# Performance work log

Measured on AMD Instinct MI355X. Metric: run time of the kernel, lower is better.

The kernel has to match this reference:

```python
import jax, jax.numpy as jnp
import numpy as np

N, D, H, L, B, DFF = 100000, 256, 8, 64, 4096, 1024
HD = D // H  # head_dim
EPS = 1e-5


def _xavier(k, shape):
    lim = (6.0 / (shape[0] + shape[1])) ** 0.5
    return jax.random.uniform(k, shape, jnp.float32, -lim, lim)


def setup_inputs() -> dict:
    key = jax.random.key(0)
    ks = jax.random.split(key, 12)
    batch = jax.random.randint(ks[0], (B,), 0, N)
    nei_idx = jax.random.randint(ks[1], (B, L), 0, N)
    # faithful to neis_ = [[k] + neighbor[k] ...]: self node is first neighbor
    nei_idx = nei_idx.at[:, 0].set(batch)
    lengths = jax.random.randint(ks[2], (B,), 1, L + 1)
    nei_mask = jnp.arange(L)[None, :] >= lengths[:, None]  # True = NaN padding
    embeddings = jax.random.normal(ks[3], (N, D), jnp.float32)
    return {
        "batch": batch, "nei_idx": nei_idx, "nei_mask": nei_mask,
        "embeddings": embeddings,
        "Wq": _xavier(ks[4], (D, D)), "bq": jnp.zeros((D,), jnp.float32),
        "Wk": _xavier(ks[5], (D, D)), "bk": jnp.zeros((D,), jnp.float32),
        "Wv": _xavier(ks[6], (D, D)), "bv": jnp.zeros((D,), jnp.float32),
        "Wo": _xavier(ks[7], (D, D)), "bo": jnp.zeros((D,), jnp.float32),
        "W1": _xavier(ks[8], (D, DFF)), "b1": jnp.zeros((DFF,), jnp.float32),
        "W2": _xavier(ks[9], (DFF, D)), "b2": jnp.zeros((D,), jnp.float32),
        "ln1_w": jnp.ones((D,), jnp.float32), "ln1_b": jnp.zeros((D,), jnp.float32),
        "ln2_w": jnp.ones((D,), jnp.float32), "ln2_b": jnp.zeros((D,), jnp.float32),
    }


def _layer_norm(y, w, b):
    mu = y.mean(-1, keepdims=True)
    var = ((y - mu) ** 2).mean(-1, keepdims=True)
    return (y - mu) / jnp.sqrt(var + EPS) * w + b


def reference(batch, nei_idx, nei_mask, embeddings,
              Wq, bq, Wk, bk, Wv, bv, Wo, bo,
              W1, b1, W2, b2, ln1_w, ln1_b, ln2_w, ln2_b):
    x = embeddings[batch]        # [B, D]  query-node embeddings
    nei = embeddings[nei_idx]    # [B, L, D] gathered (padded) neighbor embeds
    q = ((x @ Wq + bq) * (HD ** -0.5)).reshape(B, H, HD)
    k = (nei @ Wk + bk).reshape(B, L, H, HD)
    v = (nei @ Wv + bv).reshape(B, L, H, HD)
    scores = jnp.einsum('bhd,blhd->bhl', q, k)          # single-query attn
    scores = jnp.where(nei_mask[:, None, :], -jnp.inf, scores)
    att = jax.nn.softmax(scores, axis=-1)               # [B, H, L]
    attout = jnp.einsum('bhl,blhd->bhd', att, v).reshape(B, D) @ Wo + bo
    s = _layer_norm(x + attout, ln1_w, ln1_b)
    # note: original applies relu after BOTH linear1 and linear2
    f = jax.nn.relu(jax.nn.relu(s @ W1 + b1) @ W2 + b2)
    return _layer_norm(s + f, ln2_w, ln2_b)
```

## Files before the change

kernel.cpp:

```cpp
#include <hip/hip_runtime.h>
#include <hip/hip_bf16.h>
#include <math.h>

#define BQ   4096
#define D    256
#define NH   8
#define HD   32
#define LN_  64
#define DFF  1024
#define EPSV 1e-5f
#define QSCALE 0.17677669529663687f

typedef __attribute__((ext_vector_type(8))) short short8;
typedef __attribute__((ext_vector_type(4))) float f32x4;

#define ESWZ(row, byte) ((byte) ^ (((row) & 7) << 4))

__device__ __forceinline__ float wave_sum(float v){
#pragma unroll
  for (int off = 32; off; off >>= 1) v += __shfl_xor(v, off, 64);
  return v;
}
__device__ __forceinline__ unsigned short f2bf(float f){
  __hip_bfloat16 h = __float2bfloat16(f);
  unsigned short r; __builtin_memcpy(&r, &h, 2); return r;
}
__device__ __forceinline__ unsigned pk2(float a, float b){
  __hip_bfloat162 h = __float22bfloat162_rn(make_float2(a, b));
  unsigned r; __builtin_memcpy(&r, &h, 4); return r;
}

__global__ __launch_bounds__(256) void k_prep(
    const float* __restrict__ Wq, const float* __restrict__ Wk,
    const float* __restrict__ Wv, const float* __restrict__ Wo,
    const float* __restrict__ W1, const float* __restrict__ W2,
    const float* __restrict__ bq, const float* __restrict__ bv,
    const float* __restrict__ bo,
    const int* __restrict__ batch, const float* __restrict__ emb,
    const unsigned int* __restrict__ maskw,
    unsigned short* __restrict__ W1t, unsigned short* __restrict__ W2t,
    unsigned short* __restrict__ Mt, unsigned short* __restrict__ Gt,
    float* __restrict__ pb, float* __restrict__ bo2,
    float* __restrict__ X, unsigned short* __restrict__ Xb,
    int* __restrict__ flagsArr){
  __shared__ float smem[4224];
  const int bid = blockIdx.x;
  const int tid = threadIdx.x;

  if (bid < 128){
    const float* src; unsigned short* dst; int K, N, t0;
    if (bid < 64){ src = W1; dst = W1t; K = 256;  N = 1024; t0 = bid; }
    else         { src = W2; dst = W2t; K = 1024; N = 256;  t0 = bid - 64; }
    const int ntx = N / 64;
    const int k0 = (t0 / ntx) * 64, n0 = (t0 % ntx) * 64;
    float (*Ts)[65] = (float(*)[65])smem;
    {
      int r = tid >> 2, c4 = (tid & 3) * 16;
#pragma unroll
      for (int i = 0; i < 4; i++)
        *(float4*)&Ts[r][c4 + i * 4] = *(const float4*)(src + (size_t)(k0 + r) * N + n0 + c4 + i * 4);
    }
    __syncthreads();
    {
      int n = tid >> 2, kc = (tid & 3) * 16;
      unsigned int pk[8];
#pragma unroll
      for (int i = 0; i < 8; i++)
        pk[i] = pk2(Ts[kc + 2 * i][n], Ts[kc + 2 * i + 1][n]);
      unsigned short* orow = dst + (size_t)(n0 + n) * K + k0 + kc;
      *(uint4*)(orow)     = *(uint4*)&pk[0];
      *(uint4*)(orow + 8) = *(uint4*)&pk[4];
    }
    return;
  }
  if (bid < 256){
    int t0 = bid - 128;
    int hd0 = (t0 & 31) * 64, c0 = (t0 >> 5) * 64;
    int h = hd0 >> 8, d0 = hd0 & 255;
    float (*WqS)[33] = (float(*)[33])smem;
    float (*WkS)[33] = (float(*)[33])(smem + 64 * 33);
#pragma unroll
    for (int s = 0; s < 2; s++){
      int idx = tid + s * 256;
      int row = idx >> 3, c4 = (idx & 7) * 4;
      *(float4*)&WqS[row][c4] = *(const float4*)(Wq + (size_t)(c0 + row) * 256 + h * 32 + c4);
      *(float4*)&WkS[row][c4] = *(const float4*)(Wk + (size_t)(d0 + row) * 256 + h * 32 + c4);
    }
    __syncthreads();
    int jo = (tid >> 4) * 4, io = (tid & 15) * 4;
    float acc[4][4];
#pragma unroll
    for (int j = 0; j < 4; j++)
#pragma unroll
      for (int i = 0; i < 4; i++) acc[j][i] = 0.f;
#pragma unroll
    for (int t = 0; t < 32; t++){
#pragma unroll
      for (int j = 0; j < 4; j++){
        float kv = WkS[jo + j][t];
#pragma unroll
        for (int i = 0; i < 4; i++) acc[j][i] = fmaf(kv, WqS[io + i][t], acc[j][i]);
      }
    }
#pragma unroll
    for (int j = 0; j < 4; j++){
      uint2 o;
      o.x = pk2(acc[j][0] * QSCALE, acc[j][1] * QSCALE);
      o.y = pk2(acc[j][2] * QSCALE, acc[j][3] * QSCALE);
      *(uint2*)(Mt + (size_t)(hd0 + jo + j) * 256 + c0 + io) = o;
    }
    if (c0 == 0 && tid < 64){
      float s = 0.f;
#pragma unroll
      for (int t = 0; t < 32; t++) s = fmaf(WkS[tid][t], bq[h * 32 + t], s);
      pb[hd0 + tid] = s * QSCALE;
    }
    return;
  }
  if (bid < 384){
    int t0 = bid - 256;
    int hd0 = (t0 & 31) * 64, n0 = (t0 >> 5) * 64;
    int h = hd0 >> 8, d0 = hd0 & 255;
    float (*WvS)[33] = (float(*)[33])smem;
    float (*WoS)[65] = (float(*)[65])(smem + 64 * 33);
#pragma unroll
    for (int s = 0; s < 2; s++){
      int idx = tid + s * 256;
      int row = idx >> 3, c4 = (idx & 7) * 4;
      *(float4*)&WvS[row][c4] = *(const float4*)(Wv + (size_t)(d0 + row) * 256 + h * 32 + c4);
      int row2 = idx >> 4, c42 = (idx & 15) * 4;
      *(float4*)&WoS[row2][c42] = *(const float4*)(Wo + (size_t)(h * 32 + row2) * 256 + n0 + c42);
    }
    __syncthreads();
    int jo = (tid >> 4) * 4, io = (tid & 15) * 4;
    float acc[4][4];
#pragma unroll
    for (int i = 0; i < 4; i++)
#pragma unroll
      for (int j = 0; j < 4; j++) acc[i][j] = 0.f;
#pragma unroll
    for (int t = 0; t < 32; t++){
#pragma unroll
      for (int i = 0; i < 4; i++){
        float ov = WoS[t][io + i];
#pragma unroll
        for (int j = 0; j < 4; j++) acc[i][j] = fmaf(ov, WvS[jo + j][t], acc[i][j]);
      }
    }
#pragma unroll
    for (int i = 0; i < 4; i++){
      uint2 o;
      o.x = pk2(acc[i][0], acc[i][1]);
      o.y = pk2(acc[i][2], acc[i][3]);
      *(uint2*)(Gt + (size_t)(n0 + io + i) * 2048 + hd0 + jo) = o;
    }
    return;
  }
  if (bid == 384){
    int n = tid;
    float s = bo[n];
    for (int j = 0; j < 256; j++) s = fmaf(bv[j], Wo[(size_t)j * 256 + n], s);
    bo2[n] = s;
    return;
  }
  if (bid < 641){
    int* df = (int*)smem;
    if (tid == 0) df[0] = 0;
    __syncthreads();
    int idx = (bid - 385) * 256 + tid;
    unsigned int v = maskw[idx];
    int bits = 0;
    if (v == 0x3F800000u) bits = 2;
    else if (v & 0xFFFFFF00u) bits = 1;
    int b2 = __any(bits & 2) ? 2 : 0;
    int b1 = __any(bits & 1) ? 1 : 0;
    if ((tid & 63) == 0 && (b1 | b2)) atomicOr(df, b1 | b2);
    __syncthreads();
    if (tid == 0) flagsArr[bid - 385] = df[0];
    return;
  }
  {
    int gid = (bid - 641) * 256 + tid;
    int b = gid >> 6, c = gid & 63;
    float4 v = ((const float4*)(emb + (size_t)batch[b] * D))[c];
    ((float4*)(X + (size_t)b * D))[c] = v;
    uint2 p;
    p.x = pk2(v.x, v.y);
    p.y = pk2(v.z, v.w);
    ((uint2*)Xb)[gid] = p;
  }
}

template<int BM, int BN, int EPI, bool OUTBF>
__global__ __launch_bounds__(256) void k_mgemm(const unsigned short* __restrict__ A,
                                               const unsigned short* __restrict__ Bt,
                                               const float* __restrict__ bias,
                                               void* __restrict__ Cout,
                                               int M, int N, int K){
  constexpr int BK = 64;
  constexpr int WM = BM / 2, WN = BN / 2;
  constexpr int MR = WM / 16, NR = WN / 16;
  constexpr int AIT = BM * 8 / 256;
  constexpr int BIT = BN * 8 / 256;
  __shared__ __align__(16) unsigned short As[BM * BK];
  __shared__ __align__(16) unsigned short Bs[BN * BK];
  char* ab = (char*)As; char* bb = (char*)Bs;
  const int tid = threadIdx.x;
  const int w = tid >> 6, lane = tid & 63;
  const int wm = w >> 1, wn = w & 1;
  const int gx = gridDim.x;
  const int nwg = gx * gridDim.y;
  const int o = blockIdx.y * gx + blockIdx.x;
  const int lin = (o & 7) * (nwg >> 3) + (o >> 3);
  const int row0 = (lin / gx) * BM, col0 = (lin % gx) * BN;
  f32x4 acc[MR][NR];
#pragma unroll
  for (int m = 0; m < MR; m++)
#pragma unroll
    for (int n = 0; n < NR; n++) acc[m][n] = (f32x4){0.f, 0.f, 0.f, 0.f};

  for (int k0 = 0; k0 < K; k0 += BK){
#pragma unroll
    for (int s = 0; s < AIT; s++){
      int c = s * 256 + tid;
      int r = c >> 3, jj = c & 7;
      uint4 v = *(const uint4*)(A + (size_t)(row0 + r) * K + k0 + jj * 8);
      *(uint4*)(ab + ESWZ(r, r * 128 + jj * 16)) = v;
    }
#pragma unroll
    for (int s = 0; s < BIT; s++){
      int c = s * 256 + tid;
      int r = c >> 3, jj = c & 7;
      uint4 v = *(const uint4*)(Bt + (size_t)(col0 + r) * K + k0 + jj * 8);
      *(uint4*)(bb + ESWZ(r, r * 128 + jj * 16)) = v;
    }
    __syncthreads();
#pragma unroll
    for (int kk = 0; kk < 2; kk++){
      short8 af[MR], bf[NR];
#pragma unroll
      for (int m = 0; m < MR; m++){
        int r = wm * WM + m * 16 + (lane & 15);
        af[m] = *(const short8*)(ab + ESWZ(r, r * 128 + (kk * 4 + (lane >> 4)) * 16));
      }
#pragma unroll
      for (int n = 0; n < NR; n++){
        int r = wn * WN + n * 16 + (lane & 15);
        bf[n] = *(const short8*)(bb + ESWZ(r, r * 128 + (kk * 4 + (lane >> 4)) * 16));
      }
#pragma unroll
      for (int m = 0; m < MR; m++)
#pragma unroll
        for (int n = 0; n < NR; n++)
          acc[m][n] = __builtin_amdgcn_mfma_f32_16x16x32_bf16(af[m], bf[n], acc[m][n], 0, 0, 0);
    }
    __syncthreads();
  }
#pragma unroll
  for (int m = 0; m < MR; m++){
#pragma unroll
    for (int n = 0; n < NR; n++){
      int col = col0 + wn * WN + n * 16 + (lane & 15);
      float bsv = bias[col];
      int rbase = row0 + wm * WM + m * 16 + (lane >> 4) * 4;
#pragma unroll
      for (int r = 0; r < 4; r++){
        float v = acc[m][n][r] + bsv;
        if (EPI == 3) v = fmaxf(v, 0.f);
        if (OUTBF) ((unsigned short*)Cout)[(size_t)(rbase + r) * N + col] = f2bf(v);
        else       ((float*)Cout)[(size_t)(rbase + r) * N + col] = v;
      }
    }
  }
}

__global__ __launch_bounds__(256) void k_attn(const int* __restrict__ nei_idx,
                                              const void* __restrict__ nei_mask,
                                              const int* __restrict__ flagsArr,
                                              const float* __restrict__ emb,
                                              const unsigned short* __restrict__ Pb,
                                              unsigned short* __restrict__ Cb){
  const int b = blockIdx.x;
  const int tid = threadIdx.x;
  const int w = tid >> 6, lane = tid & 63;
  __shared__ __align__(16) unsigned short Ebf[64 * 256];
  __shared__ __align__(16) unsigned short Pl[9 * 256];
  __shared__ float sc[NH * LN_];
  __shared__ float mskv[LN_];
  __shared__ int   fred[4];
  char* eb = (char*)Ebf;
  char* pl = (char*)Pl;
  float* pf = (float*)Ebf;

  {
    int f = flagsArr[tid];
#pragma unroll
    for (int off = 32; off; off >>= 1) f |= __shfl_xor(f, off, 64);
    if (lane == 0) fred[w] = f;
  }
  float4 vr[16];
#pragma unroll
  for (int i = 0; i < 16; i++){
    int nid = nei_idx[(size_t)b * LN_ + w * 16 + i];
    vr[i] = ((const float4*)(emb + (size_t)nid * D))[lane];
  }
  {
    int r = tid >> 5, cb16 = (tid & 31) * 16;
    uint4 v = *(const uint4*)((const char*)Pb + (size_t)b * 4096 + r * 512 + cb16);
    *(uint4*)(pl + ESWZ(r, r * 512 + cb16)) = v;
  }
  if (tid < 64) *(uint2*)(pl + 8 * 512 + tid * 8) = make_uint2(0u, 0u);
  __syncthreads();

#pragma unroll
  for (int i = 0; i < 16; i++){
    int l = w * 16 + i;
    uint2 p;
    p.x = pk2(vr[i].x, vr[i].y);
    p.y = pk2(vr[i].z, vr[i].w);
    *(uint2*)(eb + ESWZ(l, l * 512 + lane * 8)) = p;
  }
  if (tid < LN_){
    int fl = fred[0] | fred[1] | fred[2] | fred[3];
    int mf = (fl & 2) ? 2 : ((fl & 1) ? 1 : 0);
    bool m;
    if (mf == 1)      m = ((const unsigned char*)nei_mask)[(size_t)b * LN_ + tid] != 0;
    else if (mf == 2) m = ((const float*)nei_mask)[(size_t)b * LN_ + tid] != 0.f;
    else              m = ((const int*)nei_mask)[(size_t)b * LN_ + tid] != 0;
    mskv[tid] = m ? 1.f : 0.f;
  }
  __syncthreads();

  {
    const int hr = lane & 15;
    const int arow = hr < 8 ? hr : 8;
    const int bl = w * 16 + (lane & 15);
    const int koff = (lane >> 4) * 16;
    f32x4 acc = {0.f, 0.f, 0.f, 0.f};
    __builtin_amdgcn_s_setprio(1);
#pragma unroll
    for (int kk = 0; kk < 8; kk++){
      short8 af = *(const short8*)(pl + ESWZ(arow, arow * 512 + kk * 64 + koff));
      short8 bf = *(const short8*)(eb + ESWZ(bl, bl * 512 + kk * 64 + koff));
      acc = __builtin_amdgcn_mfma_f32_16x16x32_bf16(af, bf, acc, 0, 0, 0);
    }
    __builtin_amdgcn_s_setprio(0);
    int hb = (lane >> 4) * 4;
    if (hb < 8){
#pragma unroll
      for (int r = 0; r < 4; r++) sc[(hb + r) * LN_ + bl] = acc[r];
    }
  }
  __syncthreads();

  {
    int h = tid >> 5, j = tid & 31;
    float v0 = mskv[j]      > 0.5f ? -INFINITY : sc[h * LN_ + j];
    float v1 = mskv[j + 32] > 0.5f ? -INFINITY : sc[h * LN_ + j + 32];
    float m = fmaxf(v0, v1);
#pragma unroll
    for (int off = 16; off; off >>= 1) m = fmaxf(m, __shfl_xor(m, off, 64));
    float e0 = __expf(v0 - m), e1 = __expf(v1 - m);
    float s = e0 + e1;
#pragma unroll
    for (int off = 16; off; off >>= 1) s += __shfl_xor(s, off, 64);
    float inv = 1.f / s;
    sc[h * LN_ + j]      = e0 * inv;
    sc[h * LN_ + j + 32] = e1 * inv;
  }
  __syncthreads();

  {
    float4 acc[NH];
#pragma unroll
    for (int h = 0; h < NH; h++) acc[h] = make_float4(0.f, 0.f, 0.f, 0.f);
#pragma unroll
    for (int i = 0; i < 16; i++){
      int l = w * 16 + i;
#pragma unroll
      for (int h = 0; h < NH; h++){
        float t = sc[h * LN_ + l];
        acc[h].x = fmaf(t, vr[i].x, acc[h].x);
        acc[h].y = fmaf(t, vr[i].y, acc[h].y);
        acc[h].z = fmaf(t, vr[i].z, acc[h].z);
        acc[h].w = fmaf(t, vr[i].w, acc[h].w);
      }
    }
#pragma unroll
    for (int h = 0; h < NH; h++)
      *(float4*)&pf[w * 2048 + h * 256 + lane * 4] = acc[h];
  }
  __syncthreads();

#pragma unroll
  for (int s = 0; s < 2; s++){
    int gi = tid + s * 256;
    int h = gi >> 6, d4 = gi & 63;
    float4 v0 = *(float4*)&pf[0 * 2048 + h * 256 + d4 * 4];
    float4 v1 = *(float4*)&pf[1 * 2048 + h * 256 + d4 * 4];
    float4 v2 = *(float4*)&pf[2 * 2048 + h * 256 + d4 * 4];
    float4 v3 = *(float4*)&pf[3 * 2048 + h * 256 + d4 * 4];
    float x = v0.x + v1.x + v2.x + v3.x;
    float y = v0.y + v1.y + v2.y + v3.y;
    float z = v0.z + v1.z + v2.z + v3.z;
    float u = v0.w + v1.w + v2.w + v3.w;
    uint2 o;
    o.x = pk2(x, y);
    o.y = pk2(z, u);
    *(uint2*)(Cb + (size_t)b * 2048 + h * 256 + d4 * 4) = o;
  }
}

__global__ __launch_bounds__(256) void k_ln(const float* __restrict__ A,
                                            const float* __restrict__ Bv,
                                            const float* __restrict__ w,
                                            const float* __restrict__ bi,
                                            float* __restrict__ out,
                                            unsigned short* __restrict__ outb){
  const int row = blockIdx.x, tid = threadIdx.x;
  const int wv = tid >> 6, lane = tid & 63;
  __shared__ float red[8];
  float v = A[(size_t)row * D + tid] + Bv[(size_t)row * D + tid];
  float s = wave_sum(v);
  if (lane == 0) red[wv] = s;
  __syncthreads();
  float mu = (red[0] + red[1] + red[2] + red[3]) * (1.f / D);
  float d = v - mu;
  float s2 = wave_sum(d * d);
  if (lane == 0) red[4 + wv] = s2;
  __syncthreads();
  float var = (red[4] + red[5] + red[6] + red[7]) * (1.f / D);
  float res = d * rsqrtf(var + EPSV) * w[tid] + bi[tid];
  out[(size_t)row * D + tid] = res;
  if (outb) outb[(size_t)row * D + tid] = f2bf(res);
}

extern "C" void kernel_launch(void* const* d_in, const int* in_sizes, int n_in,
                              void* d_out, int out_size, void* d_ws, size_t ws_size,
                              hipStream_t stream){
  (void)in_sizes; (void)n_in; (void)out_size; (void)ws_size;
  const int*   batch    = (const int*)d_in[0];
  const int*   nei_idx  = (const int*)d_in[1];
  const void*  nei_mask = d_in[2];
  const float* emb      = (const float*)d_in[3];
  const float* Wq = (const float*)d_in[4];  const float* bq = (const float*)d_in[5];
  const float* Wk = (const float*)d_in[6];
  const float* Wv = (const float*)d_in[8];  const float* bv = (const float*)d_in[9];
  const float* Wo = (const float*)d_in[10]; const float* bo = (const float*)d_in[11];
  const float* W1 = (const float*)d_in[12]; const float* b1 = (const float*)d_in[13];
  const float* W2 = (const float*)d_in[14]; const float* b2 = (const float*)d_in[15];
  const float* ln1w = (const float*)d_in[16]; const float* ln1b = (const float*)d_in[17];
  const float* ln2w = (const float*)d_in[18]; const float* ln2b = (const float*)d_in[19];

  float* ws = (float*)d_ws;
  float* X  = ws;
  float* Y  = ws + (size_t)1 * 1048576;
  float* S  = ws + (size_t)2 * 1048576;
  float* F  = ws + (size_t)3 * 1048576;
  unsigned short* Pbf = (unsigned short*)(ws + (size_t)4 * 1048576);
  unsigned short* Cb  = Pbf;
  unsigned short* Sb  = (unsigned short*)(ws + (size_t)8 * 1048576);
  unsigned short* HHb = (unsigned short*)(ws + (size_t)9 * 1048576);
  unsigned short* Xb  = (unsigned short*)(ws + (size_t)11 * 1048576);
  char* wb = (char*)(ws + (size_t)12 * 1048576);
  unsigned short* W1t = (unsigned short*)(wb);
  unsigned short* W2t = (unsigned short*)(wb + (512u << 10));
  unsigned short* Mt  = (unsigned short*)(wb + (1024u << 10));
  unsigned short* Gt  = (unsigned short*)(wb + (2048u << 10));
  float* pbv  = (float*)(wb + (3072u << 10));
  float* bo2  = (float*)(wb + (3072u << 10) + 8192);
  int*   flagsArr = (int*)(wb + (3072u << 10) + 16384);
  float* out = (float*)d_out;

  k_prep<<<1665, 256, 0, stream>>>(Wq, Wk, Wv, Wo, W1, W2, bq, bv, bo,
                                   batch, emb, (const unsigned int*)nei_mask,
                                   W1t, W2t, Mt, Gt, pbv, bo2, X, Xb, flagsArr);
  k_mgemm<128, 64, 2, true><<<dim3(2048 / 64, BQ / 128), 256, 0, stream>>>(Xb, Mt, pbv, Pbf, BQ, 2048, 256);
  k_attn<<<BQ, 256, 0, stream>>>(nei_idx, nei_mask, flagsArr, emb, Pbf, Cb);
  k_mgemm<32, 64, 2, false><<<dim3(D / 64, BQ / 32), 256, 0, stream>>>(Cb, Gt, bo2, Y, BQ, D, 2048);
  k_ln<<<BQ, 256, 0, stream>>>(X, Y, ln1w, ln1b, S, Sb);
  k_mgemm<128, 64, 3, true><<<dim3(DFF / 64, BQ / 128), 256, 0, stream>>>(Sb, W1t, b1, HHb, BQ, DFF, 256);
  k_mgemm<32, 64, 3, false><<<dim3(D / 64, BQ / 32), 256, 0, stream>>>(HHb, W2t, b2, F, BQ, D, DFF);
  k_ln<<<BQ, 256, 0, stream>>>(S, F, ln2w, ln2b, out, nullptr);
}
```

Baseline: 119.6 us.

## Halve attention kernel LDS by staging bf16 neighbor tile in two K-halves

The shared bf16 neighbor buffer in the attention kernel shrinks from 64x256 to 64x128. The score MFMA loop now runs in two K-halves, each half writing its bf16 columns and then synchronizing. The per-wave partial outputs are also stored as bf16 instead of fp32 so they fit in the smaller buffer. This cuts LDS per block so more blocks can be resident per CU, at the cost of extra barriers and bf16 rounding of the partial sums before the cross-wave reduction.

```diff
diff --git a/kernel.cpp b/kernel.cpp
--- a/kernel.cpp
+++ b/kernel.cpp
@@ -29,6 +29,8 @@
   __hip_bfloat162 h = __float22bfloat162_rn(make_float2(a, b));
   unsigned r; __builtin_memcpy(&r, &h, 4); return r;
 }
+__device__ __forceinline__ float bflo(unsigned u){ return __uint_as_float(u << 16); }
+__device__ __forceinline__ float bfhi(unsigned u){ return __uint_as_float(u & 0xFFFF0000u); }
 
 __global__ __launch_bounds__(256) void k_prep(
     const float* __restrict__ Wq, const float* __restrict__ Wk,
@@ -283,14 +285,14 @@
   const int b = blockIdx.x;
   const int tid = threadIdx.x;
   const int w = tid >> 6, lane = tid & 63;
-  __shared__ __align__(16) unsigned short Ebf[64 * 256];
+  __shared__ __align__(16) unsigned short EbfH[64 * 128];
   __shared__ __align__(16) unsigned short Pl[9 * 256];
   __shared__ float sc[NH * LN_];
   __shared__ float mskv[LN_];
   __shared__ int   fred[4];
-  char* eb = (char*)Ebf;
+  char* eb = (char*)EbfH;
   char* pl = (char*)Pl;
-  float* pf = (float*)Ebf;
+  unsigned* pfu = (unsigned*)EbfH;
 
   {
     int f = flagsArr[tid];
@@ -312,14 +314,6 @@
   if (tid < 64) *(uint2*)(pl + 8 * 512 + tid * 8) = make_uint2(0u, 0u);
   __syncthreads();
 
-#pragma unroll
-  for (int i = 0; i < 16; i++){
-    int l = w * 16 + i;
-    uint2 p;
-    p.x = pk2(vr[i].x, vr[i].y);
-    p.y = pk2(vr[i].z, vr[i].w);
-    *(uint2*)(eb + ESWZ(l, l * 512 + lane * 8)) = p;
-  }
   if (tid < LN_){
     int fl = fred[0] | fred[1] | fred[2] | fred[3];
     int mf = (fl & 2) ? 2 : ((fl & 1) ? 1 : 0);
@@ -329,22 +323,38 @@
     else              m = ((const int*)nei_mask)[(size_t)b * LN_ + tid] != 0;
     mskv[tid] = m ? 1.f : 0.f;
   }
-  __syncthreads();
-
-  {
-    const int hr = lane & 15;
-    const int arow = hr < 8 ? hr : 8;
-    const int bl = w * 16 + (lane & 15);
-    const int koff = (lane >> 4) * 16;
-    f32x4 acc = {0.f, 0.f, 0.f, 0.f};
+
+  f32x4 acc = {0.f, 0.f, 0.f, 0.f};
+  const int hr = lane & 15;
+  const int arow = hr < 8 ? hr : 8;
+  const int bl = w * 16 + (lane & 15);
+  const int koff = (lane >> 4) * 16;
+#pragma unroll
+  for (int half = 0; half < 2; half++){
+    if ((lane >> 5) == half){
+      int cl = lane & 31;
+#pragma unroll
+      for (int i = 0; i < 16; i++){
+        int l = w * 16 + i;
+        uint2 p;
+        p.x = pk2(vr[i].x, vr[i].y);
+        p.y = pk2(vr[i].z, vr[i].w);
+        *(uint2*)(eb + ESWZ(l, l * 256 + cl * 8)) = p;
+      }
+    }
+    __syncthreads();
     __builtin_amdgcn_s_setprio(1);
 #pragma unroll
-    for (int kk = 0; kk < 8; kk++){
-      short8 af = *(const short8*)(pl + ESWZ(arow, arow * 512 + kk * 64 + koff));
-      short8 bf = *(const short8*)(eb + ESWZ(bl, bl * 512 + kk * 64 + koff));
+    for (int kk = 0; kk < 4; kk++){
+      int kabs = half * 4 + kk;
+      short8 af = *(const short8*)(pl + ESWZ(arow, arow * 512 + kabs * 64 + koff));
+      short8 bf = *(const short8*)(eb + ESWZ(bl, bl * 256 + kk * 64 + koff));
       acc = __builtin_amdgcn_mfma_f32_16x16x32_bf16(af, bf, acc, 0, 0, 0);
     }
     __builtin_amdgcn_s_setprio(0);
+    __syncthreads();
+  }
+  {
     int hb = (lane >> 4) * 4;
     if (hb < 8){
 #pragma unroll
@@ -371,24 +381,28 @@
   __syncthreads();
 
   {
-    float4 acc[NH];
-#pragma unroll
-    for (int h = 0; h < NH; h++) acc[h] = make_float4(0.f, 0.f, 0.f, 0.f);
+    float4 pacc[NH];
+#pragma unroll
+    for (int h = 0; h < NH; h++) pacc[h] = make_float4(0.f, 0.f, 0.f, 0.f);
 #pragma unroll
     for (int i = 0; i < 16; i++){
       int l = w * 16 + i;
 #pragma unroll
       for (int h = 0; h < NH; h++){
         float t = sc[h * LN_ + l];
-        acc[h].x = fmaf(t, vr[i].x, acc[h].x);
-        acc[h].y = fmaf(t, vr[i].y, acc[h].y);
-        acc[h].z = fmaf(t, vr[i].z, acc[h].z);
-        acc[h].w = fmaf(t, vr[i].w, acc[h].w);
-      }
-    }
-#pragma unroll
-    for (int h = 0; h < NH; h++)
-      *(float4*)&pf[w * 2048 + h * 256 + lane * 4] = acc[h];
+        pacc[h].x = fmaf(t, vr[i].x, pacc[h].x);
+        pacc[h].y = fmaf(t, vr[i].y, pacc[h].y);
+        pacc[h].z = fmaf(t, vr[i].z, pacc[h].z);
+        pacc[h].w = fmaf(t, vr[i].w, pacc[h].w);
+      }
+    }
+#pragma unroll
+    for (int h = 0; h < NH; h++){
+      uint2 p;
+      p.x = pk2(pacc[h].x, pacc[h].y);
+      p.y = pk2(pacc[h].z, pacc[h].w);
+      *(uint2*)&pfu[w * 1024 + h * 128 + lane * 2] = p;
+    }
   }
   __syncthreads();
 
@@ -396,14 +410,13 @@
   for (int s = 0; s < 2; s++){
     int gi = tid + s * 256;
     int h = gi >> 6, d4 = gi & 63;
-    float4 v0 = *(float4*)&pf[0 * 2048 + h * 256 + d4 * 4];
-    float4 v1 = *(float4*)&pf[1 * 2048 + h * 256 + d4 * 4];
-    float4 v2 = *(float4*)&pf[2 * 2048 + h * 256 + d4 * 4];
-    float4 v3 = *(float4*)&pf[3 * 2048 + h * 256 + d4 * 4];
-    float x = v0.x + v1.x + v2.x + v3.x;
-    float y = v0.y + v1.y + v2.y + v3.y;
-    float z = v0.z + v1.z + v2.z + v3.z;
-    float u = v0.w + v1.w + v2.w + v3.w;
+    float x = 0.f, y = 0.f, z = 0.f, u = 0.f;
+#pragma unroll
+    for (int wv = 0; wv < 4; wv++){
+      uint2 p = *(uint2*)&pfu[wv * 1024 + h * 128 + d4 * 2];
+      x += bflo(p.x); y += bfhi(p.x);
+      z += bflo(p.y); u += bfhi(p.y);
+    }
     uint2 o;
     o.x = pk2(x, y);
     o.y = pk2(z, u);
```

New measurement: 119.6 us (median of 2 runs). About the same (-0.0%).
